# Optimization experiments

Measured on AMD Instinct MI355X. Metric: run time of the kernel, lower is better.

The kernel has to match this reference:

```python
import jax, jax.numpy as jnp
import numpy as np

EPS = 1e-12
SAMPLE_SIZES = (100, 50)  # hardcoded in the torch module


def setup_inputs() -> dict:
    key = jax.random.key(0)
    k1, k2, k3, k4 = jax.random.split(key, 4)
    N, E, C_IN, C_HID, C_OUT = 50000, 1600000, 256, 64, 128
    x = jax.random.normal(k1, (N, C_IN), dtype=jnp.float32)
    edge_index = jax.random.randint(k2, (2, E), 0, N, dtype=jnp.int64)
    W1 = jax.random.normal(k3, (C_IN, C_HID), dtype=jnp.float32) / np.sqrt(C_IN)
    b1 = jnp.zeros((C_HID,), dtype=jnp.float32)
    W2 = jax.random.normal(k4, (C_HID, C_OUT), dtype=jnp.float32) / np.sqrt(C_HID)
    b2 = jnp.zeros((C_OUT,), dtype=jnp.float32)
    return {"x": x, "edge_index": edge_index, "W1": W1, "b1": b1, "W2": W2, "b2": b2}


def _sample_mask(edge_index, num_samples, key):
    """Keep at most num_samples random out-edges per source node (fixed-shape mask)."""
    src = edge_index[0]
    E = src.shape[0]
    pri = jax.random.uniform(key, (E,))
    order = jnp.lexsort((pri, src))            # group by src, random order within group
    src_sorted = src[order]
    first = jnp.searchsorted(src_sorted, src_sorted, side="left")
    rank = jnp.arange(E) - first               # rank within each src group
    keep_sorted = rank < num_samples
    mask = jnp.zeros((E,), dtype=jnp.float32).at[order].set(keep_sorted.astype(jnp.float32))
    return mask


def _gcn_conv(x, edge_index, edge_weight, W, b, num_nodes):
    """PyG GCNConv: self-loops + symmetric deg^-1/2 normalization, aggregate at dst."""
    h = x @ W                                   # [N, out]
    src, dst = edge_index[0], edge_index[1]
    loop = jnp.arange(num_nodes, dtype=src.dtype)
    src_f = jnp.concatenate([src, loop])
    dst_f = jnp.concatenate([dst, loop])
    w_f = jnp.concatenate([edge_weight, jnp.ones((num_nodes,), dtype=edge_weight.dtype)])
    deg = jax.ops.segment_sum(w_f, dst_f, num_segments=num_nodes)
    dinv = jnp.where(deg > 0, jax.lax.rsqrt(jnp.maximum(deg, EPS)), 0.0)
    norm = w_f * dinv[src_f] * dinv[dst_f]      # [E+N]
    msgs = h[src_f] * norm[:, None]             # gather + scale (memory bound)
    out = jax.ops.segment_sum(msgs, dst_f, num_segments=num_nodes)
    return out + b


def reference(x, edge_index, W1, b1, W2, b2):
    num_nodes = x.shape[0]
    skey = jax.random.key(42)
    sk1, sk2 = jax.random.split(skey)
    m1 = _sample_mask(edge_index, SAMPLE_SIZES[0], sk1)
    m2 = _sample_mask(edge_index, SAMPLE_SIZES[1], sk2)
    h = _gcn_conv(x, edge_index, m1, W1, b1, num_nodes)
    h = jax.nn.relu(h)
    h = h / jnp.maximum(jnp.linalg.norm(h, axis=-1, keepdims=True), EPS)  # F.normalize(p=2)
    out = _gcn_conv(h, edge_index, m2, W2, b2, num_nodes)
    return out
```

## Files before the change

kernel.cpp:

```cpp
#include <hip/hip_runtime.h>

typedef unsigned int u32;
typedef unsigned short u16;
typedef unsigned long long u64;
typedef __attribute__((ext_vector_type(8))) short bh8;
typedef __attribute__((ext_vector_type(4))) float f4;

#define HMAX 1024
#define MAXD 128
#define SB_CAP 24576
#define DB_CAP 6144
#define SBCHUNK 8192
#define SPLIT 8
#define G1S 72
#define DROP_CAP 32768
#define CPAD 16

__device__ inline f4 mfma16(bh8 a, bh8 b, f4 c) {
  return __builtin_amdgcn_mfma_f32_16x16x32_bf16(a, b, c, 0, 0, 0);
}

__host__ __device__ inline void tf2x32(u32 k0, u32 k1, u32 x0, u32 x1, u32& o0, u32& o1) {
  u32 ks2 = k0 ^ k1 ^ 0x1BD11BDAu;
#define ROTL32(x,d) (((x)<<(d))|((x)>>(32-(d))))
#define TFR(r) { x0 += x1; x1 = ROTL32(x1,(r)); x1 ^= x0; }
  x0 += k0; x1 += k1;
  TFR(13) TFR(15) TFR(26) TFR(6)
  x0 += k1; x1 += ks2 + 1u;
  TFR(17) TFR(29) TFR(16) TFR(24)
  x0 += ks2; x1 += k0 + 2u;
  TFR(13) TFR(15) TFR(26) TFR(6)
  x0 += k0; x1 += k1 + 3u;
  TFR(17) TFR(29) TFR(16) TFR(24)
  x0 += k1; x1 += ks2 + 4u;
  TFR(13) TFR(15) TFR(26) TFR(6)
  x0 += ks2; x1 += k0 + 5u;
  o0 = x0; o1 = x1;
#undef TFR
#undef ROTL32
}

__device__ inline u16 f2bf(float f) {
  u32 u = __float_as_uint(f);
  return (u16)((u + 0x7FFFu + ((u >> 16) & 1u)) >> 16);
}
__device__ inline float bflo(u32 u) { return __uint_as_float(u << 16); }
__device__ inline float bfhi(u32 u) { return __uint_as_float(u & 0xFFFF0000u); }

#define ACC8(uv, wt) \
  a0 = fmaf(wt, bflo(uv.x), a0); a1 = fmaf(wt, bfhi(uv.x), a1); \
  a2 = fmaf(wt, bflo(uv.y), a2); a3 = fmaf(wt, bfhi(uv.y), a3); \
  a4 = fmaf(wt, bflo(uv.z), a4); a5 = fmaf(wt, bfhi(uv.z), a5); \
  a6 = fmaf(wt, bflo(uv.w), a6); a7 = fmaf(wt, bfhi(uv.w), a7);

#define GATHER_BURST4(TBL, BASEOFF) \
    { \
      float w0 = __shfl(wgt, grp + (BASEOFF), 64); int s0 = __shfl(s, grp + (BASEOFF), 64); \
      uint4 u0 = TBL[(size_t)s0 * 8 + lo8]; \
      float w1 = 0.f, w2 = 0.f, w3 = 0.f; uint4 u1 = u0, u2 = u0, u3 = u0; \
      if (nq > (BASEOFF)/8 + 1) { w1 = __shfl(wgt, grp + (BASEOFF) + 8, 64);  int s1 = __shfl(s, grp + (BASEOFF) + 8, 64);  u1 = TBL[(size_t)s1 * 8 + lo8]; } \
      if (nq > (BASEOFF)/8 + 2) { w2 = __shfl(wgt, grp + (BASEOFF) + 16, 64); int s2 = __shfl(s, grp + (BASEOFF) + 16, 64); u2 = TBL[(size_t)s2 * 8 + lo8]; } \
      if (nq > (BASEOFF)/8 + 3) { w3 = __shfl(wgt, grp + (BASEOFF) + 24, 64); int s3 = __shfl(s, grp + (BASEOFF) + 24, 64); u3 = TBL[(size_t)s3 * 8 + lo8]; } \
      ACC8(u0, w0) \
      if (nq > (BASEOFF)/8 + 1) { ACC8(u1, w1) } \
      if (nq > (BASEOFF)/8 + 2) { ACC8(u2, w2) } \
      if (nq > (BASEOFF)/8 + 3) { ACC8(u3, w3) } \
    }

struct BinS { u32 lsrc[128]; u32 lbase[128]; u32 ldst[512]; u32 dbase[512]; };
struct GemS { u16 xs[64 * G1S]; u16 ws[64 * G1S]; };

__global__ __launch_bounds__(256) void k_mega1(const int* __restrict__ ei, int E,
                                               const float* __restrict__ x, int N,
                                               const float* __restrict__ W1, const float* __restrict__ W2,
                                               int* __restrict__ srcCnt, u32* __restrict__ srcRec,
                                               int* __restrict__ dstCnt, u64* __restrict__ dstRec,
                                               u16* __restrict__ h1b, u16* __restrict__ W2t, int nBin) {
  __shared__ __align__(16) char smem[sizeof(GemS)];
  int t = threadIdx.x;
  int bid = blockIdx.x;
  int nGemm = (N + 63) >> 6;

  if (bid < nBin) {
    BinS& S = *(BinS*)smem;
    if (t < 128) S.lsrc[t] = 0;
    for (int v = t; v < 512; v += 256) S.ldst[v] = 0;
    __syncthreads();
    int lo = bid * SBCHUNK;
    int hi = min(lo + SBCHUNK, E);
    bool fast = ((E & 3) == 0);

    auto loadE = [&](int e0, int nv, int* sv, int* dv) {
      if (nv == 8 && fast) {
        int4 a0 = *((const int4*)(ei + e0));
        int4 a1 = *((const int4*)(ei + e0 + 4));
        int4 b0 = *((const int4*)(ei + E + e0));
        int4 b1 = *((const int4*)(ei + E + e0 + 4));
        sv[0]=a0.x; sv[1]=a0.y; sv[2]=a0.z; sv[3]=a0.w; sv[4]=a1.x; sv[5]=a1.y; sv[6]=a1.z; sv[7]=a1.w;
        dv[0]=b0.x; dv[1]=b0.y; dv[2]=b0.z; dv[3]=b0.w; dv[4]=b1.x; dv[5]=b1.y; dv[6]=b1.z; dv[7]=b1.w;
      } else {
        for (int j = 0; j < nv; ++j) { sv[j] = ei[e0 + j]; dv[j] = ei[E + e0 + j]; }
      }
    };

    for (int sub = 0; sub < SBCHUNK; sub += 2048) {
      int e0 = lo + sub + 8 * t;
      int nv = min(8, hi - e0); if (nv < 0) nv = 0;
      int sv[8], dv[8];
      loadE(e0, nv, sv, dv);
      for (int j = 0; j < nv; ++j) {
        atomicAdd(&S.lsrc[sv[j] >> 9], 1u);
        atomicAdd(&S.ldst[dv[j] >> 7], 1u);
      }
    }
    __syncthreads();
    if (t < 128) {
      u32 c = S.lsrc[t];
      if (c) S.lbase[t] = (u32)atomicAdd(&srcCnt[t * CPAD], (int)c);
      S.lsrc[t] = 0;
    }
    for (int v = t; v < 512; v += 256) {
      u32 cd = S.ldst[v];
      if (cd) S.dbase[v] = (u32)atomicAdd(&dstCnt[v * CPAD], (int)cd);
      S.ldst[v] = 0;
    }
    __syncthreads();
    for (int sub = 0; sub < SBCHUNK; sub += 2048) {
      int e0 = lo + sub + 8 * t;
      int nv = min(8, hi - e0); if (nv < 0) nv = 0;
      int sv[8], dv[8];
      loadE(e0, nv, sv, dv);
      for (int j = 0; j < nv; ++j) {
        int s = sv[j], d = dv[j];
        u32 i = (u32)(e0 + j);
        int bs = s >> 9;
        u32 slot = S.lbase[bs] + atomicAdd(&S.lsrc[bs], 1u);
        if (slot < SB_CAP) srcRec[(size_t)bs * SB_CAP + slot] = ((u32)(s & 511) << 21) | i;
        int bd = d >> 7;
        u32 slot2 = S.dbase[bd] + atomicAdd(&S.ldst[bd], 1u);
        if (slot2 < DB_CAP)
          dstRec[(size_t)bd * DB_CAP + slot2] = ((u64)(d & 127) << 37) | ((u64)(u32)s << 21) | i;
      }
    }
  } else if (bid < nBin + nGemm) {
    GemS& G = *(GemS*)smem;
    int wv = t >> 6, lane = t & 63;
    int qd = lane >> 4, md = lane & 15;
    int m0 = (bid - nBin) * 64;
    if (m0 >= N) return;
    f4 acc[4] = {};
    for (int ks = 0; ks < 256; ks += 64) {
      __syncthreads();
#pragma unroll
      for (int i = 0; i < 4; ++i) {
        int f = t + 256 * i;
        int r = f >> 4, c4 = f & 15;
        int grow = m0 + r; if (grow >= N) grow = N - 1;
        float4 v = ((const float4*)x)[(size_t)grow * 64 + (ks >> 2) + c4];
        u32 p0 = (u32)f2bf(v.x) | ((u32)f2bf(v.y) << 16);
        u32 p1 = (u32)f2bf(v.z) | ((u32)f2bf(v.w) << 16);
        *((uint2*)(G.xs + r * G1S + c4 * 4)) = make_uint2(p0, p1);
      }
#pragma unroll
      for (int i = 0; i < 4; ++i) {
        int f = t + 256 * i;
        int k = f >> 4, c4 = f & 15;
        float4 v = ((const float4*)W1)[(ks + k) * 16 + c4];
        int n0 = c4 * 4;
        G.ws[(n0 + 0) * G1S + k] = f2bf(v.x);
        G.ws[(n0 + 1) * G1S + k] = f2bf(v.y);
        G.ws[(n0 + 2) * G1S + k] = f2bf(v.z);
        G.ws[(n0 + 3) * G1S + k] = f2bf(v.w);
      }
      __syncthreads();
#pragma unroll
      for (int kk = 0; kk < 64; kk += 32) {
        bh8 af = *((const bh8*)(G.xs + (16 * wv + md) * G1S + kk + qd * 8));
#pragma unroll
        for (int nt = 0; nt < 4; ++nt) {
          bh8 bf = *((const bh8*)(G.ws + (nt * 16 + md) * G1S + kk + qd * 8));
          acc[nt] = mfma16(af, bf, acc[nt]);
        }
      }
    }
#pragma unroll
    for (int nt = 0; nt < 4; ++nt)
#pragma unroll
      for (int r = 0; r < 4; ++r) {
        int row = m0 + 16 * wv + qd * 4 + r;
        if (row < N) h1b[(size_t)row * 64 + nt * 16 + md] = f2bf(acc[nt][r]);
      }
  } else {
    for (int e = t; e < 64 * 128; e += 256) {
      int n = e & 127, k = e >> 7;
      W2t[n * 64 + k] = f2bf(W2[k * 128 + n]);
    }
  }
}

__global__ __launch_bounds__(256) void k_shist(const int* __restrict__ srcCnt, const u32* __restrict__ srcRec,
                                               int* __restrict__ outdegB) {
  int bk = blockIdx.x >> 3;
  int part = blockIdx.x & (SPLIT - 1);
  int total = min(srcCnt[bk * CPAD], SB_CAP);
  int lo = total * part / SPLIT;
  int hi = total * (part + 1) / SPLIT;
  __shared__ u32 cnt[512];
  int t = threadIdx.x;
  cnt[t] = 0; cnt[t + 256] = 0;
  __syncthreads();
  const u32* R = srcRec + (size_t)bk * SB_CAP;
  for (int i = lo + t; i < hi; i += 256) atomicAdd(&cnt[R[i] >> 21], 1u);
  __syncthreads();
  int base = bk * 512;
  for (int v = t; v < 512; v += 256) {
    u32 c = cnt[v];
    if (c) atomicAdd(&outdegB[base + v], (int)c);
  }
}

__global__ __launch_bounds__(256) void k_hdetect(const int* __restrict__ outdegB, u32* __restrict__ idAB,
                                                 int* __restrict__ hcA, int* __restrict__ hcB,
                                                 const int* __restrict__ dstCnt, int* __restrict__ bucketBase,
                                                 int* __restrict__ dptr, int nbD, int N) {
  int t = threadIdx.x;
  if (blockIdx.x == 0) {
    __shared__ int sc[512], tp[512];
    for (int i = t; i < 512; i += 256) sc[i] = (i < nbD) ? min(dstCnt[i * CPAD], DB_CAP) : 0;
    __syncthreads();
    for (int off = 1; off < 512; off <<= 1) {
      for (int i = t; i < 512; i += 256) tp[i] = sc[i] + ((i >= off) ? sc[i - off] : 0);
      __syncthreads();
      for (int i = t; i < 512; i += 256) sc[i] = tp[i];
      __syncthreads();
    }
    for (int i = t; i < 512; i += 256) {
      if (i < nbD) bucketBase[i] = (i == 0) ? 0 : sc[i - 1];
    }
    if (t == 0) {
      int tot = sc[nbD - 1];
      bucketBase[nbD] = tot;
      dptr[N] = tot;
    }
  }
  int v = blockIdx.x * 256 + t;
  if (v >= N) return;
  int dg = outdegB[v];
  u32 pk = 0;
  if (dg > 50) {
    int idb = atomicAdd(hcB, 1);
    if (idb < HMAX) pk = (u32)(idb + 1);
    if (dg > 100) {
      int ida = atomicAdd(hcA, 1);
      if (ida < HMAX) pk |= (u32)(ida + 1) << 16;
    }
  }
  idAB[v] = pk;
}

__global__ __launch_bounds__(256) void k_hfill(const int* __restrict__ srcCnt, const u32* __restrict__ srcRec,
                                               const u32* __restrict__ idAB,
                                               int* __restrict__ bcA, u64* __restrict__ bukA,
                                               int* __restrict__ bcB, u64* __restrict__ bukB,
                                               u32 kaA, u32 kbA, u32 kaB, u32 kbB) {
  int bk = blockIdx.x >> 3;
  int part = blockIdx.x & (SPLIT - 1);
  int total = min(srcCnt[bk * CPAD], SB_CAP);
  int lo = total * part / SPLIT;
  int hi = total * (part + 1) / SPLIT;
  const u32* R = srcRec + (size_t)bk * SB_CAP;
  int base = bk * 512;
  for (int i = lo + threadIdx.x; i < hi; i += 256) {
    u32 r = R[i];
    u32 pk = idAB[base + (int)(r >> 21)];
    if (pk) {
      u32 e = r & 0x1FFFFFu;
      int idb = (int)(pk & 0xFFFFu) - 1;
      if (idb >= 0) {
        u32 w0, w1; tf2x32(kaB, kbB, 0u, e, w0, w1);
        int slot = atomicAdd(&bcB[idb], 1);
        if (slot < MAXD) bukB[(size_t)idb * MAXD + slot] = ((u64)((w0 ^ w1) >> 9) << 32) | e;
      }
      int ida = (int)(pk >> 16) - 1;
      if (ida >= 0) {
        u32 w0, w1; tf2x32(kaA, kbA, 0u, e, w0, w1);
        int slot = atomicAdd(&bcA[ida], 1);
        if (slot < MAXD) bukA[(size_t)ida * MAXD + slot] = ((u64)((w0 ^ w1) >> 9) << 32) | e;
      }
    }
  }
}

__global__ __launch_bounds__(256) void k_rank2(const int* __restrict__ hcA, const int* __restrict__ bcA,
                                               const u64* __restrict__ bukA,
                                               const int* __restrict__ hcB, const int* __restrict__ bcB,
                                               const u64* __restrict__ bukB,
                                               int* __restrict__ dropCnt, u32* __restrict__ dropList) {
  bool isA = blockIdx.x < (HMAX / 4);
  int bx = isA ? blockIdx.x : blockIdx.x - HMAX / 4;
  const int* hcount = isA ? hcA : hcB;
  const int* bcount = isA ? bcA : bcB;
  const u64* bucket = isA ? bukA : bukB;
  int S = isA ? 100 : 50;
  u32 bit = isA ? 1u : 2u;
  int wid = (bx * 256 + (int)threadIdx.x) >> 6;
  int lane = threadIdx.x & 63;
  int hc = hcount[0]; if (hc > HMAX) hc = HMAX;
  if (wid >= hc) return;
  int d = bcount[wid]; if (d > MAXD) d = MAXD;
  const u64* B = bucket + (size_t)wid * MAXD;
  for (int i = lane; i < d; i += 64) {
    u64 ki = B[i];
    int rank = 0;
    for (int j = 0; j < d; ++j) rank += (B[j] < ki) ? 1 : 0;
    if (rank >= S) {
      int idx = atomicAdd(dropCnt, 1);
      if (idx < DROP_CAP) dropList[idx] = ((u32)ki & 0x1FFFFFu) | (bit << 21);
    }
  }
}

__global__ __launch_bounds__(256) void k_phase2(const int* __restrict__ bucketBase,
                                                const int* __restrict__ dstCnt,
                                                const u64* __restrict__ dstRec,
                                                const int* __restrict__ dropCnt,
                                                const u32* __restrict__ dropList,
                                                u32* __restrict__ entries, int* __restrict__ dptr,
                                                float* __restrict__ dinv1, float* __restrict__ dinv2, int N) {
  int b = blockIdx.x;
  int base = bucketBase[b];
  int cnt0 = min(dstCnt[b * CPAD], DB_CAP);
  const u64* R = dstRec + (size_t)b * DB_CAP;
  __shared__ u32 cnt[128];
  __shared__ u32 htab[4096];
  __shared__ u32 ws2[2];
  __shared__ u32 earr[DB_CAP];
  int t = threadIdx.x;
  if (t < 128) cnt[t] = 0;
  for (int i = t; i < 4096; i += 256) htab[i] = 0xFFFFFFFFu;
  __syncthreads();
  int dc = min(dropCnt[0], 3072);
  for (int i = t; i < dc; i += 256) {
    u32 pk = dropList[i];
    u32 key = pk & 0x1FFFFFu;
    u32 h = (key * 2654435761u) >> 20;
    while (true) {
      u32 old = atomicCAS(&htab[h], 0xFFFFFFFFu, pk);
      if (old == 0xFFFFFFFFu) break;
      if ((old & 0x1FFFFFu) == key) { atomicOr(&htab[h], pk & 0x00600000u); break; }
      h = (h + 1) & 4095;
    }
  }
  __syncthreads();
  for (int i = t; i < cnt0; i += 256) {
    u64 r = R[i];
    u32 dl = (u32)(r >> 37) & 127u;
    u32 key = (u32)r & 0x1FFFFFu;
    u32 drop = 0;
    u32 h = (key * 2654435761u) >> 20;
    while (true) {
      u32 v = htab[h];
      if (v == 0xFFFFFFFFu) break;
      if ((v & 0x1FFFFFu) == key) { drop = (v >> 21) & 3u; break; }
      h = (h + 1) & 4095;
    }
    u32 src = (u32)(r >> 21) & 0xFFFFu;
    earr[i] = src | (drop << 16) | (dl << 18);
    u32 add = 1u + ((1u - (drop & 1u)) << 10) + ((1u - ((drop >> 1) & 1u)) << 20);
    atomicAdd(&cnt[dl], add);
  }
  __syncthreads();
  u32 c0 = (t < 128) ? cnt[t] : 0;
  u32 tot = c0 & 1023u;
  int lane = t & 63, w = t >> 6;
  u32 incl = tot;
  for (int off = 1; off < 64; off <<= 1) {
    u32 nbv = (u32)__shfl_up((int)incl, off, 64);
    if (lane >= off) incl += nbv;
  }
  if (lane == 63 && w == 0) ws2[0] = incl;
  __syncthreads();
  u32 excl = incl - tot + ((w == 1) ? ws2[0] : 0u);
  int v0 = b * 128 + t;
  if (t < 128 && v0 < N) {
    dptr[v0] = base + (int)excl;
    dinv1[v0] = 1.0f / sqrtf((float)(((c0 >> 10) & 1023u) + 1u));
    dinv2[v0] = 1.0f / sqrtf((float)(((c0 >> 20) & 1023u) + 1u));
  }
  __syncthreads();
  if (t < 128) cnt[t] = excl;
  __syncthreads();
  for (int i = t; i < cnt0; i += 256) {
    u32 p = earr[i];
    u32 dl = (p >> 18) & 127u;
    u32 drop = (p >> 16) & 3u;
    u32 src = p & 0xFFFFu;
    u32 slot = atomicAdd(&cnt[dl], 1u);
    entries[base + slot] = src | ((drop & 1u) ? 0u : (1u << 30)) | ((drop & 2u) ? 0u : (1u << 31));
  }
}

__global__ __launch_bounds__(256) void k_conv1n(const int* __restrict__ ptr, const u32* __restrict__ entries,
                                                const float* __restrict__ dinv1, const uint4* __restrict__ h1q,
                                                const float* __restrict__ b1, uint4* __restrict__ hnbq, int N) {
  int wid = (blockIdx.x * 256 + threadIdx.x) >> 6;
  if (wid >= N) return;
  int lane = threadIdx.x & 63;
  int lo8 = lane & 7, grp = lane >> 3;
  int beg = ptr[wid], end = ptr[wid + 1];
  float a0 = 0.f, a1 = 0.f, a2 = 0.f, a3 = 0.f, a4 = 0.f, a5 = 0.f, a6 = 0.f, a7 = 0.f;
  for (int cb = beg; cb < end; cb += 64) {
    int idx = cb + lane;
    float wgt = 0.f; int s = 0;
    if (idx < end) {
      u32 e = entries[idx];
      s = (int)(e & 0xFFFFu);
      if (e & (1u << 30)) wgt = dinv1[s];
    }
    int nq = (min(64, end - cb) + 7) >> 3;
    GATHER_BURST4(h1q, 0)
    if (nq > 4) { GATHER_BURST4(h1q, 32) }
  }
#pragma unroll
  for (int off = 8; off < 64; off <<= 1) {
    a0 += __shfl_xor(a0, off, 64); a1 += __shfl_xor(a1, off, 64);
    a2 += __shfl_xor(a2, off, 64); a3 += __shfl_xor(a3, off, 64);
    a4 += __shfl_xor(a4, off, 64); a5 += __shfl_xor(a5, off, 64);
    a6 += __shfl_xor(a6, off, 64); a7 += __shfl_xor(a7, off, 64);
  }
  float dv = dinv1[wid];
  uint4 uo = h1q[(size_t)wid * 8 + lo8];
  a0 = fmaf(dv, bflo(uo.x), a0); a1 = fmaf(dv, bfhi(uo.x), a1);
  a2 = fmaf(dv, bflo(uo.y), a2); a3 = fmaf(dv, bfhi(uo.y), a3);
  a4 = fmaf(dv, bflo(uo.z), a4); a5 = fmaf(dv, bfhi(uo.z), a5);
  a6 = fmaf(dv, bflo(uo.w), a6); a7 = fmaf(dv, bfhi(uo.w), a7);
  float4 bbA = ((const float4*)b1)[lo8 * 2];
  float4 bbB = ((const float4*)b1)[lo8 * 2 + 1];
  float o0 = fmaxf(fmaf(dv, a0, bbA.x), 0.f);
  float o1 = fmaxf(fmaf(dv, a1, bbA.y), 0.f);
  float o2 = fmaxf(fmaf(dv, a2, bbA.z), 0.f);
  float o3 = fmaxf(fmaf(dv, a3, bbA.w), 0.f);
  float o4 = fmaxf(fmaf(dv, a4, bbB.x), 0.f);
  float o5 = fmaxf(fmaf(dv, a5, bbB.y), 0.f);
  float o6 = fmaxf(fmaf(dv, a6, bbB.z), 0.f);
  float o7 = fmaxf(fmaf(dv, a7, bbB.w), 0.f);
  float ss = fmaf(o0, o0, fmaf(o1, o1, fmaf(o2, o2, o3 * o3)))
           + fmaf(o4, o4, fmaf(o5, o5, fmaf(o6, o6, o7 * o7)));
#pragma unroll
  for (int off = 1; off < 8; off <<= 1) ss += __shfl_xor(ss, off, 8);
  float sc = 1.f / fmaxf(sqrtf(ss), 1e-12f);
  if (lane < 8) {
    uint4 pv;
    pv.x = (u32)f2bf(o0 * sc) | ((u32)f2bf(o1 * sc) << 16);
    pv.y = (u32)f2bf(o2 * sc) | ((u32)f2bf(o3 * sc) << 16);
    pv.z = (u32)f2bf(o4 * sc) | ((u32)f2bf(o5 * sc) << 16);
    pv.w = (u32)f2bf(o6 * sc) | ((u32)f2bf(o7 * sc) << 16);
    hnbq[(size_t)wid * 8 + lo8] = pv;
  }
}

__global__ __launch_bounds__(256) void k_agg2(const int* __restrict__ ptr, const u32* __restrict__ entries,
                                              const float* __restrict__ dinv2, const uint4* __restrict__ hnq,
                                              uint4* __restrict__ agg2q, int N) {
  int wid = (blockIdx.x * 256 + threadIdx.x) >> 6;
  if (wid >= N) return;
  int lane = threadIdx.x & 63;
  int lo8 = lane & 7, grp = lane >> 3;
  int beg = ptr[wid], end = ptr[wid + 1];
  float a0 = 0.f, a1 = 0.f, a2 = 0.f, a3 = 0.f, a4 = 0.f, a5 = 0.f, a6 = 0.f, a7 = 0.f;
  for (int cb = beg; cb < end; cb += 64) {
    int idx = cb + lane;
    float wgt = 0.f; int s = 0;
    if (idx < end) {
      u32 e = entries[idx];
      s = (int)(e & 0xFFFFu);
      if (e & (1u << 31)) wgt = dinv2[s];
    }
    int nq = (min(64, end - cb) + 7) >> 3;
    GATHER_BURST4(hnq, 0)
    if (nq > 4) { GATHER_BURST4(hnq, 32) }
  }
#pragma unroll
  for (int off = 8; off < 64; off <<= 1) {
    a0 += __shfl_xor(a0, off, 64); a1 += __shfl_xor(a1, off, 64);
    a2 += __shfl_xor(a2, off, 64); a3 += __shfl_xor(a3, off, 64);
    a4 += __shfl_xor(a4, off, 64); a5 += __shfl_xor(a5, off, 64);
    a6 += __shfl_xor(a6, off, 64); a7 += __shfl_xor(a7, off, 64);
  }
  float dv = dinv2[wid];
  uint4 uo = hnq[(size_t)wid * 8 + lo8];
  a0 = fmaf(dv, bflo(uo.x), a0); a1 = fmaf(dv, bfhi(uo.x), a1);
  a2 = fmaf(dv, bflo(uo.y), a2); a3 = fmaf(dv, bfhi(uo.y), a3);
  a4 = fmaf(dv, bflo(uo.z), a4); a5 = fmaf(dv, bfhi(uo.z), a5);
  a6 = fmaf(dv, bflo(uo.w), a6); a7 = fmaf(dv, bfhi(uo.w), a7);
  if (lane < 8) {
    uint4 pv;
    pv.x = (u32)f2bf(dv * a0) | ((u32)f2bf(dv * a1) << 16);
    pv.y = (u32)f2bf(dv * a2) | ((u32)f2bf(dv * a3) << 16);
    pv.z = (u32)f2bf(dv * a4) | ((u32)f2bf(dv * a5) << 16);
    pv.w = (u32)f2bf(dv * a6) | ((u32)f2bf(dv * a7) << 16);
    agg2q[(size_t)wid * 8 + lo8] = pv;
  }
}

#define G2S 72
__global__ __launch_bounds__(256) void k_gemm2f(const u16* __restrict__ aggb, const u16* __restrict__ W2t,
                                                const float* __restrict__ b2, float* __restrict__ out, int N) {
  __shared__ u16 hs[64 * G2S];
  __shared__ u16 ws[128 * G2S];
  int t = threadIdx.x;
  int wv = t >> 6, lane = t & 63;
  int qd = lane >> 4, md = lane & 15;
  int m0 = blockIdx.x * 64;
#pragma unroll
  for (int i = 0; i < 2; ++i) {
    int cc = t + 256 * i;
    int r = cc >> 3, kc = (cc & 7) * 8;
    int grow = m0 + r; if (grow >= N) grow = N - 1;
    *((uint4*)(hs + r * G2S + kc)) = *((const uint4*)(aggb + (size_t)grow * 64 + kc));
  }
#pragma unroll
  for (int i = 0; i < 4; ++i) {
    int cc = t + 256 * i;
    int n = cc >> 3, kc = (cc & 7) * 8;
    *((uint4*)(ws + n * G2S + kc)) = *((const uint4*)(W2t + n * 64 + kc));
  }
  __syncthreads();
  f4 acc[8] = {};
#pragma unroll
  for (int kk = 0; kk < 64; kk += 32) {
    bh8 af = *((const bh8*)(hs + (16 * wv + md) * G2S + kk + qd * 8));
#pragma unroll
    for (int nt = 0; nt < 8; ++nt) {
      bh8 bf = *((const bh8*)(ws + (nt * 16 + md) * G2S + kk + qd * 8));
      acc[nt] = mfma16(af, bf, acc[nt]);
    }
  }
#pragma unroll
  for (int nt = 0; nt < 8; ++nt) {
    float bv = b2[nt * 16 + md];
#pragma unroll
    for (int r = 0; r < 4; ++r) {
      int row = m0 + 16 * wv + qd * 4 + r;
      if (row < N) out[(size_t)row * 128 + nt * 16 + md] = acc[nt][r] + bv;
    }
  }
}

extern "C" void kernel_launch(void* const* d_in, const int* in_sizes, int n_in,
                              void* d_out, int out_size, void* d_ws, size_t ws_size,
                              hipStream_t stream) {
  const float* x  = (const float*)d_in[0];
  const int*   ei = (const int*)d_in[1];
  const float* W1 = (const float*)d_in[2];
  const float* b1 = (const float*)d_in[3];
  const float* W2 = (const float*)d_in[4];
  const float* b2 = (const float*)d_in[5];
  const int N = in_sizes[0] / 256;
  const int E = in_sizes[1] / 2;
  const int nbS = (N + 511) >> 9;
  const int nbD = (N + 127) >> 7;

  u32 sk1a, sk1b, sk2a, sk2b;
  tf2x32(0u, 42u, 0u, 0u, sk1a, sk1b);
  tf2x32(0u, 42u, 0u, 1u, sk2a, sk2b);

  char* p = (char*)d_ws;
  auto alloc = [&](size_t bytes) { char* r = p; p += (bytes + 255) & ~(size_t)255; return r; };
  int* dstCnt      = (int*)alloc((size_t)512 * CPAD * 4);
  int* srcCnt      = (int*)alloc((size_t)128 * CPAD * 4);
  int* hcbA        = (int*)alloc((size_t)(1 + HMAX) * 4);
  int* hcbB        = (int*)alloc((size_t)(1 + HMAX) * 4);
  int* outdegB     = (int*)alloc((size_t)nbS * 512 * 4);
  int* dropCnt     = (int*)alloc(256);
  char* zero_end = p;
  u32* dropList = (u32*)alloc((size_t)DROP_CAP * 4);
  u32* idAB     = (u32*)alloc((size_t)nbS * 512 * 4);
  u16* h1b      = (u16*)alloc((size_t)N * 64 * 2);
  u16* hnb      = (u16*)alloc((size_t)N * 64 * 2);
  u16* agg2b    = (u16*)alloc((size_t)N * 64 * 2);
  float* dinv1  = (float*)alloc((size_t)N * 4);
  float* dinv2  = (float*)alloc((size_t)N * 4);
  int* dptr     = (int*)alloc((size_t)(N + 1) * 4);
  int* bucketBase = (int*)alloc(513 * 4);
  u32* entries  = (u32*)alloc((size_t)E * 4);
  u32* srcRec   = (u32*)alloc((size_t)nbS * SB_CAP * 4);
  u64* dstRec   = (u64*)alloc((size_t)nbD * DB_CAP * 8);
  u64* bukA     = (u64*)alloc((size_t)HMAX * MAXD * 8);
  u64* bukB     = (u64*)alloc((size_t)HMAX * MAXD * 8);
  u16* W2t      = (u16*)alloc(64 * 128 * 2);

  int* hcA = hcbA; int* bcA = hcbA + 1;
  int* hcB = hcbB; int* bcB = hcbB + 1;

  hipMemsetAsync(dstCnt, 0x00, (size_t)(zero_end - (char*)dstCnt), stream);

  const int nBin = (E + SBCHUNK - 1) / SBCHUNK;
  const int nGemm = (N + 63) / 64;
  k_mega1<<<nBin + nGemm + 1, 256, 0, stream>>>(ei, E, x, N, W1, W2,
                                                srcCnt, srcRec, dstCnt, dstRec, h1b, W2t, nBin);
  k_shist<<<nbS * SPLIT, 256, 0, stream>>>(srcCnt, srcRec, outdegB);
  k_hdetect<<<(N + 255) / 256, 256, 0, stream>>>(outdegB, idAB, hcA, hcB, dstCnt, bucketBase,
                                                 dptr, nbD, N);
  k_hfill<<<nbS * SPLIT, 256, 0, stream>>>(srcCnt, srcRec, idAB, bcA, bukA, bcB, bukB,
                                           sk1a, sk1b, sk2a, sk2b);
  k_rank2<<<HMAX / 2, 256, 0, stream>>>(hcA, bcA, bukA, hcB, bcB, bukB, dropCnt, dropList);
  k_phase2<<<nbD, 256, 0, stream>>>(bucketBase, dstCnt, dstRec, dropCnt, dropList,
                                    entries, dptr, dinv1, dinv2, N);
  k_conv1n<<<(N * 64 + 255) / 256, 256, 0, stream>>>(dptr, entries, dinv1, (const uint4*)h1b, b1,
                                                     (uint4*)hnb, N);
  k_agg2<<<(N * 64 + 255) / 256, 256, 0, stream>>>(dptr, entries, dinv2, (const uint4*)hnb,
                                                   (uint4*)agg2b, N);
  k_gemm2f<<<(N + 63) / 64, 256, 0, stream>>>(agg2b, W2t, b2, (float*)d_out, N);
}
```

Measured before the change: 255.4 us.

## Stage dst-bucket records in LDS before writing them out contiguously

The binning phase now splits each chunk into two halves. Destination records are first grouped by bucket in shared memory, using a prefix scan over the 512 bucket counts, and then written to global memory in bucket order. The aim is to replace scattered 8-byte writes across 512 buckets with more contiguous, coalesced stores. In exchange it adds a 512-entry scan with many barriers, a 32KB staging buffer that raises LDS use and may lower occupancy for the GEMM blocks, and global atomics issued twice per chunk.

New measurement: 259.3 us. Within noise of the previous version (+1.5%).

```diff
diff --git a/kernel.cpp b/kernel.cpp
--- a/kernel.cpp
+++ b/kernel.cpp
@@ -67,8 +67,14 @@
       if (nq > (BASEOFF)/8 + 3) { ACC8(u3, w3) } \
     }
 
-struct BinS { u32 lsrc[128]; u32 lbase[128]; u32 ldst[512]; u32 dbase[512]; };
+struct BinS2 {
+  u32 lsrc[128]; u32 lbase[128];
+  u32 ldst[512]; u32 dbase[512];
+  u32 lstart[512]; u32 cur[512];
+  u64 stage[4096];
+};
 struct GemS { u16 xs[64 * G1S]; u16 ws[64 * G1S]; };
+#define SMEM_BYTES ((sizeof(BinS2) > sizeof(GemS)) ? sizeof(BinS2) : sizeof(GemS))
 
 __global__ __launch_bounds__(256) void k_mega1(const int* __restrict__ ei, int E,
                                                const float* __restrict__ x, int N,
@@ -76,16 +82,13 @@
                                                int* __restrict__ srcCnt, u32* __restrict__ srcRec,
                                                int* __restrict__ dstCnt, u64* __restrict__ dstRec,
                                                u16* __restrict__ h1b, u16* __restrict__ W2t, int nBin) {
-  __shared__ __align__(16) char smem[sizeof(GemS)];
+  __shared__ __align__(16) char smem[SMEM_BYTES];
   int t = threadIdx.x;
   int bid = blockIdx.x;
   int nGemm = (N + 63) >> 6;
 
   if (bid < nBin) {
-    BinS& S = *(BinS*)smem;
-    if (t < 128) S.lsrc[t] = 0;
-    for (int v = t; v < 512; v += 256) S.ldst[v] = 0;
-    __syncthreads();
+    BinS2& S = *(BinS2*)smem;
     int lo = bid * SBCHUNK;
     int hi = min(lo + SBCHUNK, E);
     bool fast = ((E & 3) == 0);
@@ -103,44 +106,75 @@
       }
     };
 
-    for (int sub = 0; sub < SBCHUNK; sub += 2048) {
-      int e0 = lo + sub + 8 * t;
-      int nv = min(8, hi - e0); if (nv < 0) nv = 0;
-      int sv[8], dv[8];
-      loadE(e0, nv, sv, dv);
-      for (int j = 0; j < nv; ++j) {
-        atomicAdd(&S.lsrc[sv[j] >> 9], 1u);
-        atomicAdd(&S.ldst[dv[j] >> 7], 1u);
-      }
-    }
-    __syncthreads();
-    if (t < 128) {
-      u32 c = S.lsrc[t];
-      if (c) S.lbase[t] = (u32)atomicAdd(&srcCnt[t * CPAD], (int)c);
-      S.lsrc[t] = 0;
-    }
-    for (int v = t; v < 512; v += 256) {
-      u32 cd = S.ldst[v];
-      if (cd) S.dbase[v] = (u32)atomicAdd(&dstCnt[v * CPAD], (int)cd);
-      S.ldst[v] = 0;
-    }
-    __syncthreads();
-    for (int sub = 0; sub < SBCHUNK; sub += 2048) {
-      int e0 = lo + sub + 8 * t;
-      int nv = min(8, hi - e0); if (nv < 0) nv = 0;
-      int sv[8], dv[8];
-      loadE(e0, nv, sv, dv);
-      for (int j = 0; j < nv; ++j) {
-        int s = sv[j], d = dv[j];
-        u32 i = (u32)(e0 + j);
-        int bs = s >> 9;
-        u32 slot = S.lbase[bs] + atomicAdd(&S.lsrc[bs], 1u);
-        if (slot < SB_CAP) srcRec[(size_t)bs * SB_CAP + slot] = ((u32)(s & 511) << 21) | i;
-        int bd = d >> 7;
-        u32 slot2 = S.dbase[bd] + atomicAdd(&S.ldst[bd], 1u);
-        if (slot2 < DB_CAP)
-          dstRec[(size_t)bd * DB_CAP + slot2] = ((u64)(d & 127) << 37) | ((u64)(u32)s << 21) | i;
-      }
+    for (int h = 0; h < 2; ++h) {
+      int hlo = lo + h * 4096;
+      if (hlo >= hi) break;
+      int hhi = min(hlo + 4096, hi);
+      if (t < 128) S.lsrc[t] = 0;
+      for (int v = t; v < 512; v += 256) S.ldst[v] = 0;
+      __syncthreads();
+      for (int sub = 0; sub < 4096; sub += 2048) {
+        int e0 = hlo + sub + 8 * t;
+        int nv = min(8, hhi - e0); if (nv < 0) nv = 0;
+        int sv[8], dv[8];
+        loadE(e0, nv, sv, dv);
+        for (int j = 0; j < nv; ++j) {
+          atomicAdd(&S.lsrc[sv[j] >> 9], 1u);
+          atomicAdd(&S.ldst[dv[j] >> 7], 1u);
+        }
+      }
+      __syncthreads();
+      if (t < 128) {
+        u32 c = S.lsrc[t];
+        if (c) S.lbase[t] = (u32)atomicAdd(&srcCnt[t * CPAD], (int)c);
+        S.lsrc[t] = 0;
+      }
+      for (int v = t; v < 512; v += 256) {
+        u32 cd = S.ldst[v];
+        if (cd) S.dbase[v] = (u32)atomicAdd(&dstCnt[v * CPAD], (int)cd);
+      }
+      for (int v = t; v < 512; v += 256) S.lstart[v] = S.ldst[v];
+      __syncthreads();
+      {
+        u32* sb = S.lstart; u32* db = S.cur;
+        for (int off = 1; off < 512; off <<= 1) {
+          for (int v = t; v < 512; v += 256)
+            db[v] = sb[v] + ((v >= off) ? sb[v - off] : 0u);
+          __syncthreads();
+          u32* tmp = sb; sb = db; db = tmp;
+        }
+      }
+      int tot = (int)S.cur[511];
+      __syncthreads();
+      for (int v = t; v < 512; v += 256) S.lstart[v] = (v == 0) ? 0u : S.cur[v - 1];
+      __syncthreads();
+      for (int v = t; v < 512; v += 256) S.cur[v] = S.lstart[v];
+      __syncthreads();
+      for (int sub = 0; sub < 4096; sub += 2048) {
+        int e0 = hlo + sub + 8 * t;
+        int nv = min(8, hhi - e0); if (nv < 0) nv = 0;
+        int sv[8], dv[8];
+        loadE(e0, nv, sv, dv);
+        for (int j = 0; j < nv; ++j) {
+          int s = sv[j], d = dv[j];
+          u32 i = (u32)(e0 + j);
+          int bs = s >> 9;
+          u32 slot = S.lbase[bs] + atomicAdd(&S.lsrc[bs], 1u);
+          if (slot < SB_CAP) srcRec[(size_t)bs * SB_CAP + slot] = ((u32)(s & 511) << 21) | i;
+          int bd = d >> 7;
+          u32 r = atomicAdd(&S.cur[bd], 1u);
+          S.stage[r] = ((u64)(u32)bd << 45) | ((u64)(d & 127) << 37) | ((u64)(u32)s << 21) | i;
+        }
+      }
+      __syncthreads();
+      for (int i2 = t; i2 < tot; i2 += 256) {
+        u64 rec = S.stage[i2];
+        u32 bd = (u32)(rec >> 45) & 511u;
+        u32 gslot = S.dbase[bd] + ((u32)i2 - S.lstart[bd]);
+        if (gslot < DB_CAP)
+          dstRec[(size_t)bd * DB_CAP + gslot] = rec & 0x1FFFFFFFFFFFULL;
+      }
+      __syncthreads();
     }
   } else if (bid < nBin + nGemm) {
     GemS& G = *(GemS*)smem;
```
